# Kernel tuning notes

Measured on AMD Instinct MI355X. Metric: run time of the kernel, lower is better.

Reference implementation:

```python
import jax, jax.numpy as jnp
import numpy as np
from jax import lax

N = 63        # fixed by ConvTranspose chain: 3->5->9->17->33->63
ML = 3        # smoother mid channels
KS = 7        # smoother kernel size
MID = 32      # hypernet mid channels
K_ITERS = 5   # outer solver iterations
B = 256


def _conv2d(x, w, pad):
    return lax.conv_general_dilated(x, w, (1, 1), [(pad, pad), (pad, pad)],
                                    dimension_numbers=('NCHW', 'OIHW', 'NCHW'))


def _batch_conv2d(x, kernels):
    # per-sample 3x3 stencil conv via grouped conv: x [B,1,m,m], kernels [B,1,3,3]
    b, _, m1, m2 = x.shape
    out = lax.conv_general_dilated(x.reshape(1, b, m1, m2), kernels, (1, 1),
                                   [(0, 0), (0, 0)],
                                   dimension_numbers=('NCHW', 'OIHW', 'NCHW'),
                                   feature_group_count=b)
    return out.reshape(b, 1, m1 - 2, m2 - 2)


def _conv_transpose2d(x, w, b, stride, padding):
    # torch ConvTranspose2d: w layout [in, out, k, k]
    k = w.shape[-1]
    w2 = jnp.flip(w, (-2, -1)).transpose(1, 0, 2, 3)  # [out, in, k, k]
    p = k - 1 - padding
    y = lax.conv_general_dilated(x, w2, (1, 1), [(p, p), (p, p)],
                                 lhs_dilation=(stride, stride),
                                 dimension_numbers=('NCHW', 'OIHW', 'NCHW'))
    return y + b[None, :, None, None]


def _pad_bc(x):
    # F.pad (1,0,1,0) with 0 then (0,1,0,1) with 1
    x = jnp.pad(x, ((0, 0), (0, 0), (1, 0), (1, 0)))
    return jnp.pad(x, ((0, 0), (0, 0), (0, 1), (0, 1)), constant_values=1.0)


def _gelu(x):
    return jax.nn.gelu(x, approximate=False)  # torch nn.GELU default is exact


def setup_inputs() -> dict:
    key = jax.random.key(0)
    ks = jax.random.split(key, 24)
    s = 0.02
    d = {}
    d['x'] = jax.random.normal(ks[0], (B, 1, N, N), jnp.float32)
    d['f'] = jax.random.normal(ks[1], (B, 1, N, N), jnp.float32)
    d['kernelA'] = jax.random.normal(ks[2], (B, 1, 3, 3), jnp.float32)
    # smoother hypernetwork (two Linear(9->100->mL*ks*ks) stacks)
    d['fc1_w1'] = jax.random.normal(ks[3], (9, 100), jnp.float32) * s
    d['fc1_b1'] = jnp.zeros((100,), jnp.float32)
    d['fc1_w2'] = jax.random.normal(ks[4], (100, ML * KS * KS), jnp.float32) * s
    d['fc1_b2'] = jnp.zeros((ML * KS * KS,), jnp.float32)
    d['fc2_w1'] = jax.random.normal(ks[5], (9, 100), jnp.float32) * s
    d['fc2_b1'] = jnp.zeros((100,), jnp.float32)
    d['fc2_w2'] = jax.random.normal(ks[6], (100, ML * KS * KS), jnp.float32) * s
    d['fc2_b2'] = jnp.zeros((ML * KS * KS,), jnp.float32)
    # CNNFNS meta: 5 ConvTranspose2d layers (torch weight layout [in,out,k,k])
    d['ct1_w'] = jax.random.normal(ks[7], (1, MID, 3, 3), jnp.float32) * s
    d['ct1_b'] = jnp.zeros((MID,), jnp.float32)
    d['ct2_w'] = jax.random.normal(ks[8], (MID, MID, 3, 3), jnp.float32) * s
    d['ct2_b'] = jnp.zeros((MID,), jnp.float32)
    d['ct3_w'] = jax.random.normal(ks[9], (MID, MID, 3, 3), jnp.float32) * s
    d['ct3_b'] = jnp.zeros((MID,), jnp.float32)
    d['ct4_w'] = jax.random.normal(ks[10], (MID, MID, 3, 3), jnp.float32) * s
    d['ct4_b'] = jnp.zeros((MID,), jnp.float32)
    d['ct5_w'] = jax.random.normal(ks[11], (MID, 2, 3, 3), jnp.float32) * s
    d['ct5_b'] = jnp.zeros((2,), jnp.float32)
    return d


def reference(x, f, kernelA,
              fc1_w1, fc1_b1, fc1_w2, fc1_b2,
              fc2_w1, fc2_b1, fc2_w2, fc2_b2,
              ct1_w, ct1_b, ct2_w, ct2_b, ct3_w, ct3_b, ct4_w, ct4_b, ct5_w, ct5_b):
    bsz = x.shape[0]

    # --- hypernet weights depend only on kernelA: hoist out of the K loop ---
    flatA = kernelA.reshape(bsz, 9)
    w1 = (_gelu(flatA @ fc1_w1 + fc1_b1) @ fc1_w2 + fc1_b2).reshape(bsz, ML, 1, KS, KS)
    w2 = (_gelu(flatA @ fc2_w1 + fc2_b1) @ fc2_w2 + fc2_b2).reshape(bsz, 1, ML, KS, KS)

    h = _gelu(_conv_transpose2d(kernelA, ct1_w, ct1_b, 2, 1))
    h = _gelu(_conv_transpose2d(h, ct2_w, ct2_b, 2, 1))
    h = _gelu(_conv_transpose2d(h, ct3_w, ct3_b, 2, 1))
    h = _gelu(_conv_transpose2d(h, ct4_w, ct4_b, 2, 1))
    h = _conv_transpose2d(h, ct5_w, ct5_b, 2, 2)          # [B,2,N,N]
    hw = h.reshape(bsz, 1, N, N, 2)                        # memory-reinterp view as in torch
    wc = lax.complex(hw[..., 0], hw[..., 1])               # [B,1,N,N] complex

    def residual(xc):
        return f - _batch_conv2d(_pad_bc(xc), kernelA)

    def smoother(xc):
        r = residual(xc)
        def per(r_i, a_i, b_i):
            t = _conv2d(r_i[None], a_i, KS // 2)           # [1,ML,N,N]
            return _conv2d(t, b_i, KS // 2)[0]             # [1,N,N]
        g2 = jax.vmap(per)(r, w1, w2)
        return xc + g2

    def h_correct(r):
        r_hat = jnp.fft.fft2(r, norm='ortho')
        out_ft = r_hat * wc
        # torch irfft2(s=(N,N)) trims last dim to N//2+1
        return jnp.fft.irfft2(out_ft[..., : N // 2 + 1], s=(N, N), norm='ortho')

    for _ in range(K_ITERS):
        x = smoother(x)
        x = x + h_correct(residual(x))
    r = residual(x)
    return jnp.linalg.norm(r) / bsz
```

## Files before the change

kernel.cpp:

```cpp
#include <hip/hip_runtime.h>
#include <math.h>

#define NB   256
#define ND   63
#define NN   3969
#define WST  1028

__device__ __forceinline__ float gelu_f(float v){
    return 0.5f * v * (1.0f + erff(v * 0.70710678118654752440f));
}

#define FMA4(A, W, S) { (A).x=fmaf((W).x,(S),(A).x); (A).y=fmaf((W).y,(S),(A).y); \
                        (A).z=fmaf((W).z,(S),(A).z); (A).w=fmaf((W).w,(S),(A).w); }

union F4  { float4 v;    float a[4];  };
union W16 { float4 v[4]; float a[16]; };

__device__ __forceinline__ float4 gelu4(const F4& x){
    float4 r;
    r.x = gelu_f(x.a[0]); r.y = gelu_f(x.a[1]);
    r.z = gelu_f(x.a[2]); r.w = gelu_f(x.a[3]);
    return r;
}

__device__ __forceinline__ int dec_base(int uc, int H){
    int h2 = H >> 1;
    return (uc < h2) ? 4*uc : (uc < H) ? 4*(uc - h2) + 1 : 2*H;
}

template<int SIN, int SOUT, int OST, int NT>
__device__ __forceinline__ void ct_quad_stage(const float* __restrict__ cin,
                                              float* __restrict__ cout,
                                              const float* __restrict__ wb,
                                              const float* __restrict__ bsv,
                                              int tid){
    const int H  = (SOUT - 1) >> 1;
    const int UX = H + 1;
    const int NU = UX * UX * 8;
    for (int u = tid; u < NU; u += NT){
        const int cell = u >> 3, q = u & 7;
        const int ucy = cell / UX, ucx = cell - ucy*UX;
        const int oy = dec_base(ucy, H), ox = dec_base(ucx, H);
        const bool vx = (ox + 2 <= 2*H), vy = (oy + 2 <= 2*H);
        int nky, kyA[2], iyA[2];
        if (oy & 1){ nky=2; kyA[0]=0; iyA[0]=(oy+1)>>1; kyA[1]=2; iyA[1]=(oy-1)>>1; }
        else       { nky=1; kyA[0]=1; iyA[0]=oy>>1; kyA[1]=1; iyA[1]=0; }
        int nkx, kxA[2], ixA[2];
        if (ox & 1){ nkx=2; kxA[0]=0; ixA[0]=(ox+1)>>1; kxA[1]=2; ixA[1]=(ox-1)>>1; }
        else       { nkx=1; kxA[0]=1; ixA[0]=ox>>1; kxA[1]=1; ixA[1]=0; }
        F4 a00, a01, a10, a11;
        a00.v = ((const float4*)bsv)[q]; a01.v = a00.v; a10.v = a00.v; a11.v = a00.v;
        for (int yi = 0; yi < nky; yi++)
        for (int xi = 0; xi < nkx; xi++){
            const float* wp  = wb + (kyA[yi]*3 + kxA[xi])*WST + 4*q;
            const float* p00 = cin + (iyA[yi]*SIN + ixA[xi])*36;
            const float* p01 = p00 + 36;
            const float* p10 = p00 + SIN*36;
            const float* p11 = p10 + 36;
            #pragma unroll
            for (int g = 0; g < 8; g++){
                F4 i00, i01, i10, i11;
                i00.v = *(const float4*)(p00 + 4*g);
                i01.v = *(const float4*)(p01 + 4*g);
                i10.v = *(const float4*)(p10 + 4*g);
                i11.v = *(const float4*)(p11 + 4*g);
                #pragma unroll
                for (int cc = 0; cc < 4; cc++){
                    float4 w = *(const float4*)(wp + (4*g + cc)*32);
                    FMA4(a00.v, w, i00.a[cc]);
                    FMA4(a01.v, w, i01.a[cc]);
                    FMA4(a10.v, w, i10.a[cc]);
                    FMA4(a11.v, w, i11.a[cc]);
                }
            }
        }
        float4 g00 = gelu4(a00), g01 = gelu4(a01), g10 = gelu4(a10), g11 = gelu4(a11);
        size_t base = (size_t)(oy*SOUT + ox)*OST + 4*q;
        *(float4*)(cout + base) = g00;
        if (vx)        *(float4*)(cout + base + 2*(size_t)OST) = g01;
        if (vy)        *(float4*)(cout + base + 2*(size_t)SOUT*OST) = g10;
        if (vx && vy)  *(float4*)(cout + base + 2*(size_t)(SOUT+1)*OST) = g11;
    }
}

__global__ __launch_bounds__(1024)
__attribute__((amdgpu_waves_per_eu(4, 4)))
void k_ct1234(const float* __restrict__ kA,
              const float* __restrict__ cw1,
              const float* __restrict__ cw2,
              const float* __restrict__ cw3,
              const float* __restrict__ cw4,
              const float* __restrict__ b1,
              const float* __restrict__ b2,
              const float* __restrict__ b3,
              const float* __restrict__ b4,
              float* __restrict__ c4out,
              float* __restrict__ acc){
    __shared__ __align__(16) float wbuf[9*WST];
    __shared__ __align__(16) float w1s[9*36];
    __shared__ __align__(16) float c1s[31*36];
    __shared__ __align__(16) float c2s[91*36];
    __shared__ __align__(16) float c3s[307*36];
    __shared__ float b1s[32], b2s[32], b3s[32], b4s[32];
    const int b = blockIdx.x, tid = threadIdx.x;
    if (b == 0 && tid == 0) acc[0] = 0.f;
    for (int i = tid; i < 9216; i += 1024){
        int ci = i / 288, co = (i / 9) & 31, tap = i % 9;
        wbuf[tap*WST + ci*32 + co] = cw2[i];
    }
    if (tid < 288) w1s[(tid % 9)*36 + tid/9] = cw1[tid];
    if (tid < 32){ b1s[tid]=b1[tid]; b2s[tid]=b2[tid]; b3s[tid]=b3[tid]; b4s[tid]=b4[tid]; }
    __syncthreads();
    if (tid < 200){
        int px = tid >> 3, q = tid & 7;
        int oy = px / 5, ox = px % 5;
        F4 a4; a4.v = ((const float4*)b1s)[q];
        int nky, kyA[2], iyA[2];
        if (oy & 1){ nky=2; kyA[0]=0; iyA[0]=(oy+1)/2; kyA[1]=2; iyA[1]=(oy-1)/2; }
        else       { nky=1; kyA[0]=1; iyA[0]=oy/2; kyA[1]=1; iyA[1]=0; }
        int nkx, kxA[2], ixA[2];
        if (ox & 1){ nkx=2; kxA[0]=0; ixA[0]=(ox+1)/2; kxA[1]=2; ixA[1]=(ox-1)/2; }
        else       { nkx=1; kxA[0]=1; ixA[0]=ox/2; kxA[1]=1; ixA[1]=0; }
        const float* ab = kA + b*9;
        for (int yi = 0; yi < nky; yi++)
        for (int xi = 0; xi < nkx; xi++){
            float v = ab[iyA[yi]*3 + ixA[xi]];
            float4 w = *(const float4*)(w1s + (kyA[yi]*3 + kxA[xi])*36 + 4*q);
            FMA4(a4.v, w, v);
        }
        *(float4*)(c1s + px*36 + 4*q) = gelu4(a4);
    }
    __syncthreads();
    ct_quad_stage<5, 9, 36, 1024>(c1s, c2s, wbuf, b2s, tid);
    __syncthreads();
    for (int i = tid; i < 9216; i += 1024){
        int ci = i / 288, co = (i / 9) & 31, tap = i % 9;
        wbuf[tap*WST + ci*32 + co] = cw3[i];
    }
    __syncthreads();
    ct_quad_stage<9, 17, 36, 1024>(c2s, c3s, wbuf, b3s, tid);
    __syncthreads();
    for (int i = tid; i < 9216; i += 1024){
        int ci = i / 288, co = (i / 9) & 31, tap = i % 9;
        wbuf[tap*WST + ci*32 + co] = cw4[i];
    }
    __syncthreads();
    ct_quad_stage<17, 33, 32, 1024>(c3s, c4out + (size_t)b*(1089*32), wbuf, b4s, tid);
}

__global__ __launch_bounds__(512) void k_solve(const float* __restrict__ x0g,
                                               const float* __restrict__ f,
                                               const float* __restrict__ kAg,
                                               const float* __restrict__ w1a, const float* __restrict__ b1a,
                                               const float* __restrict__ w2a, const float* __restrict__ b2a,
                                               const float* __restrict__ w1b, const float* __restrict__ b1b,
                                               const float* __restrict__ w2b, const float* __restrict__ b2b,
                                               const float* __restrict__ cw5,
                                               const float* __restrict__ b5,
                                               const float* __restrict__ c4g,
                                               float* __restrict__ accg){
    __shared__ __align__(16) float xs[65*68 + 8];
    __shared__ __align__(16) float U[17152 + 8];
    __shared__ __align__(16) float Fs_r[32*68 + 8];
    __shared__ __align__(16) float Fs_i[32*68 + 8];
    __shared__ __align__(16) float vcs[4096];
    __shared__ float ws5b[9*68];
    __shared__ float w1s[148], w2s[148], dvs[64], ds_r[32], ds_i[32], red[8], hs[100];
    const int b = blockIdx.x, tid = threadIdx.x;
    float* rs  = U;
    float* tc0 = U + 4288;
    float* tc1 = U + 8576;
    float* tc2 = U + 12864;
    float*  rP  = U;
    const float4* rP4 = (const float4*)U;
    float2* TtC = (float2*)(U + 4352);
    float2* MC2 = (float2*)(U + 8448);
    float4* CC4 = (float4*)(U + 12544);
    float* c5s = U;
    const float4* F4r = (const float4*)Fs_r;
    const float4* F4i = (const float4*)Fs_i;
    const float4* vc4s = (const float4*)vcs;
    const float* fg = f + (size_t)b*NN;
    float ka[9];
    #pragma unroll
    for (int i = 0; i < 9; i++) ka[i] = kAg[b*9 + i];

    for (int i = tid; i < 2176; i += 512){
        int r = i / 68, c = i % 68;
        float vr = 0.f, vi = 0.f;
        if (c < 63){
            int m = (r * c) % 63;
            float ang = 6.283185307179586f * (float)m / 63.0f;
            vr = cosf(ang); vi = -sinf(ang);
        }
        Fs_r[i] = vr; Fs_i[i] = vi;
    }
    for (int i = tid; i < 4428; i += 512){
        int r = i / 68, c = i - r*68;
        bool interior = (r >= 1 && r <= 63 && c >= 4 && c <= 66);
        if (!interior) xs[i] = (r == 64 || c == 67) ? 1.f : 0.f;
    }
    for (int i = tid; i < 576; i += 512){
        int ci = i / 18, co = (i / 9) & 1, tap = i % 9;
        ws5b[tap*68 + ci*2 + co] = cw5[i];
    }
    for (int i = tid; i < NN; i += 512) xs[(i/ND + 1)*68 + (i%ND) + 4] = x0g[(size_t)b*NN + i];
    if (tid < 100){
        float s = b1a[tid];
        #pragma unroll
        for (int i = 0; i < 9; i++) s = fmaf(ka[i], w1a[i*100 + tid], s);
        hs[tid] = gelu_f(s);
    }
    __syncthreads();
    if (tid < 147){
        float s = b2a[tid];
        for (int k = 0; k < 100; k++) s = fmaf(hs[k], w2a[k*147 + tid], s);
        w1s[tid] = s;
    }
    __syncthreads();
    if (tid < 100){
        float s = b1b[tid];
        #pragma unroll
        for (int i = 0; i < 9; i++) s = fmaf(ka[i], w1b[i*100 + tid], s);
        hs[tid] = gelu_f(s);
    }
    __syncthreads();
    if (tid < 147){
        float s = b2b[tid];
        for (int k = 0; k < 100; k++) s = fmaf(hs[k], w2b[k*147 + tid], s);
        w2s[tid] = s;
    }
    {
        const float* ib = c4g + (size_t)b * (1089*32);
        float bb0 = b5[0], bb1 = b5[1];
        for (int p = tid; p < NN; p += 512){
            int oy = p / ND, ox = p % ND;
            float a0 = bb0, a1 = bb1;
            int nky, kyA[2], iyA[2];
            if ((oy & 1) == 0){ nky=2; kyA[0]=0; iyA[0]=oy/2+1; kyA[1]=2; iyA[1]=oy/2; }
            else              { nky=1; kyA[0]=1; iyA[0]=(oy+1)/2; kyA[1]=1; iyA[1]=0; }
            int nkx, kxA[2], ixA[2];
            if ((ox & 1) == 0){ nkx=2; kxA[0]=0; ixA[0]=ox/2+1; kxA[1]=2; ixA[1]=ox/2; }
            else              { nkx=1; kxA[0]=1; ixA[0]=(ox+1)/2; kxA[1]=1; ixA[1]=0; }
            for (int yi = 0; yi < nky; yi++)
            for (int xi = 0; xi < nkx; xi++){
                const float* ip = ib + ((size_t)iyA[yi]*33 + ixA[xi])*32;
                const float* wp = ws5b + (kyA[yi]*3 + kxA[xi])*68;
                #pragma unroll
                for (int g = 0; g < 8; g++){
                    F4 iv; iv.v = *(const float4*)(ip + 4*g);
                    #pragma unroll
                    for (int q = 0; q < 4; q++){
                        int ci = 4*g + q;
                        a0 = fmaf(iv.a[q], wp[ci*2],   a0);
                        a1 = fmaf(iv.a[q], wp[ci*2+1], a1);
                    }
                }
            }
            c5s[p]      = a0;
            c5s[NN + p] = a1;
        }
    }
    __syncthreads();
    {
        const float sc = 1.0f / 3969.0f;
        float4* vout = (float4*)vcs;
        for (int i = tid; i < 1024; i += 512){
            int ky = i >> 5, ct2 = i & 31;
            float4 o;
            #pragma unroll
            for (int j = 0; j < 2; j++){
                int kx = 2*ct2 + j;
                float re = 0.f, im = 0.f;
                if (kx <= 31){ int o2 = 2*(ky*ND + kx); re = c5s[o2]*sc; im = c5s[o2+1]*sc; }
                else if (kx <= 62){
                    int sy = (ND - ky) % ND, sx = ND - kx;
                    int o2 = 2*(sy*ND + sx); re = c5s[o2]*sc; im = -c5s[o2+1]*sc;
                }
                if (j == 0){ o.x = re; o.y = im; } else { o.z = re; o.w = im; }
            }
            vout[i] = o;
        }
        if (tid < 32){
            float2 d = {0.f, 0.f};
            if (tid >= 1){
                int iA = (ND - tid) * ND, iB = tid * ND;
                d.x = (c5s[2*iA]     - c5s[2*iB])     * sc;
                d.y = (c5s[2*iA + 1] + c5s[2*iB + 1]) * sc;
            }
            ((float2*)dvs)[tid] = d;
        }
    }
    __syncthreads();

    const int kt = tid >> 4, cg = tid & 15;
    const bool act = tid < 504;
    const int y0 = tid >> 3, xc = 8*(tid & 7);

    for (int it = 0; it < 5; it++){
        if (act){
            float racc[8] = {};
            #pragma unroll
            for (int dy = 0; dy < 3; dy++){
                W16 w;
                const float4* rp = (const float4*)(xs + (y0 + dy)*68 + xc);
                w.v[0]=rp[0]; w.v[1]=rp[1]; w.v[2]=rp[2]; w.v[3]=rp[3];
                #pragma unroll
                for (int dx = 0; dx < 3; dx++){
                    float kv = ka[dy*3 + dx];
                    #pragma unroll
                    for (int t = 0; t < 8; t++) racc[t] = fmaf(kv, w.a[3 + t + dx], racc[t]);
                }
            }
            int nw = 63 - xc; if (nw > 8) nw = 8;
            const float* fr_ = fg + y0*ND + xc;
            for (int t = 0; t < nw; t++) rs[y0*68 + 3 + xc + t] = fr_[t] - racc[t];
        }
        for (int i = tid; i < 1276; i += 512){
            int buf = i / 319, j = i - buf*319;
            float* base = U + buf*4288;
            int idx;
            if (j < 315){ int rr = j/5, cc = j - rr*5; idx = rr*68 + ((cc < 3) ? cc : 63 + cc); }
            else idx = 4284 + (j - 315);
            base[idx] = 0.f;
        }
        __syncthreads();
        if (act){
            float A0[8] = {}, A1[8] = {}, A2[8] = {};
            for (int dy = 0; dy < 7; dy++){
                int ry = y0 + dy - 3;
                if (ry < 0 || ry >= 63) continue;
                W16 w16;
                const float4* rp = (const float4*)(rs + ry*68 + xc);
                w16.v[0]=rp[0]; w16.v[1]=rp[1]; w16.v[2]=rp[2]; w16.v[3]=rp[3];
                #pragma unroll
                for (int dx = 0; dx < 7; dx++){
                    float w0 = w1s[dy*7 + dx];
                    float w1 = w1s[49 + dy*7 + dx];
                    float w2 = w1s[98 + dy*7 + dx];
                    #pragma unroll
                    for (int t = 0; t < 8; t++){
                        float v = w16.a[t+dx];
                        A0[t] = fmaf(w0, v, A0[t]);
                        A1[t] = fmaf(w1, v, A1[t]);
                        A2[t] = fmaf(w2, v, A2[t]);
                    }
                }
            }
            int nw = 63 - xc; if (nw > 8) nw = 8;
            for (int t = 0; t < nw; t++){
                int o = y0*68 + 3 + xc + t;
                tc0[o] = A0[t]; tc1[o] = A1[t]; tc2[o] = A2[t];
            }
        }
        __syncthreads();
        if (act){
            float acc2[8] = {};
            #pragma unroll
            for (int c = 0; c < 3; c++){
                const float* tcc = (c == 0) ? tc0 : (c == 1) ? tc1 : tc2;
                for (int dy = 0; dy < 7; dy++){
                    int ry = y0 + dy - 3;
                    if (ry < 0 || ry >= 63) continue;
                    W16 w16;
                    const float4* tp = (const float4*)(tcc + ry*68 + xc);
                    w16.v[0]=tp[0]; w16.v[1]=tp[1]; w16.v[2]=tp[2]; w16.v[3]=tp[3];
                    #pragma unroll
                    for (int dx = 0; dx < 7; dx++){
                        float wv = w2s[c*49 + dy*7 + dx];
                        #pragma unroll
                        for (int t = 0; t < 8; t++) acc2[t] = fmaf(wv, w16.a[t+dx], acc2[t]);
                    }
                }
            }
            int nw = 63 - xc; if (nw > 8) nw = 8;
            for (int t = 0; t < nw; t++) xs[(y0+1)*68 + 4 + xc + t] += acc2[t];
        }
        __syncthreads();
        if (act){
            float racc[8] = {};
            #pragma unroll
            for (int dy = 0; dy < 3; dy++){
                W16 w;
                const float4* rp = (const float4*)(xs + (y0 + dy)*68 + xc);
                w.v[0]=rp[0]; w.v[1]=rp[1]; w.v[2]=rp[2]; w.v[3]=rp[3];
                #pragma unroll
                for (int dx = 0; dx < 3; dx++){
                    float kv = ka[dy*3 + dx];
                    #pragma unroll
                    for (int t = 0; t < 8; t++) racc[t] = fmaf(kv, w.a[3 + t + dx], racc[t]);
                }
            }
            float out[8];
            #pragma unroll
            for (int t = 0; t < 8; t++){
                int ci = xc + t; if (ci > 62) ci = 62;
                float fv = fg[y0*ND + ci];
                out[t] = (xc + t < 63) ? (fv - racc[t]) : 0.f;
            }
            *(float4*)(rP + y0*68 + xc)     = make_float4(out[0],out[1],out[2],out[3]);
            *(float4*)(rP + y0*68 + xc + 4) = make_float4(out[4],out[5],out[6],out[7]);
        }
        __syncthreads();
        {
            float tr0,ti0=0.f,tr1,ti1=0.f,tr2,ti2=0.f,tr3,ti3=0.f;
            { F4 rv; rv.v = rP4[cg]; tr0=rv.a[0]; tr1=rv.a[1]; tr2=rv.a[2]; tr3=rv.a[3]; }
            #define A_PAIR(MM, JJ) { \
                F4 r1, r2; \
                r1.v = rP4[(MM)*17 + cg]; \
                r2.v = rP4[(63-(MM))*17 + cg]; \
                float fr = f4r.a[JJ], fi = f4i.a[JJ]; \
                float S0=r1.a[0]+r2.a[0], D0=r1.a[0]-r2.a[0]; \
                float S1=r1.a[1]+r2.a[1], D1=r1.a[1]-r2.a[1]; \
                float S2=r1.a[2]+r2.a[2], D2=r1.a[2]-r2.a[2]; \
                float S3=r1.a[3]+r2.a[3], D3=r1.a[3]-r2.a[3]; \
                tr0 = fmaf(fr, S0, tr0); ti0 = fmaf(fi, D0, ti0); \
                tr1 = fmaf(fr, S1, tr1); ti1 = fmaf(fi, D1, ti1); \
                tr2 = fmaf(fr, S2, tr2); ti2 = fmaf(fi, D2, ti2); \
                tr3 = fmaf(fr, S3, tr3); ti3 = fmaf(fi, D3, ti3); }
            {
                F4 f4r, f4i; f4r.v = F4r[kt*17]; f4i.v = F4i[kt*17];
                A_PAIR(1, 1) A_PAIR(2, 2) A_PAIR(3, 3)
            }
            for (int mq = 1; mq < 8; mq++){
                F4 f4r, f4i;
                f4r.v = F4r[kt*17 + mq];
                f4i.v = F4i[kt*17 + mq];
                A_PAIR(4*mq + 0, 0) A_PAIR(4*mq + 1, 1)
                A_PAIR(4*mq + 2, 2) A_PAIR(4*mq + 3, 3)
            }
            #undef A_PAIR
            const int c0 = 4*cg;
            TtC[(c0+0)*32 + ((kt + c0 + 0) & 31)] = make_float2(tr0, ti0);
            TtC[(c0+1)*32 + ((kt + c0 + 1) & 31)] = make_float2(tr1, ti1);
            TtC[(c0+2)*32 + ((kt + c0 + 2) & 31)] = make_float2(tr2, ti2);
            TtC[(c0+3)*32 + ((kt + c0 + 3) & 31)] = make_float2(tr3, ti3);
        }
        {
            float R0r,R0i,R1r,R1i,R2r,R2i,R3r,R3i;
            {
                float2 T0 = TtC[kt & 31];
                R0r = T0.x; R0i = T0.y;
                R1r = T0.x; R1i = T0.y;
                R2r = T0.x; R2i = T0.y;
                R3r = T0.x; R3i = T0.y;
            }
            for (int np = 1; np <= 31; np++){
                int n2 = 63 - np;
                float2 T1 = TtC[np*32 + ((kt + np) & 31)];
                float2 T2 = TtC[n2*32 + ((kt + n2) & 31)];
                F4 fr, fi;
                fr.v = F4r[np*17 + cg];
                fi.v = F4i[np*17 + cg];
                float Sx = T1.x + T2.x, Dx = T1.x - T2.x;
                float Sy = T1.y + T2.y, Dy = T2.y - T1.y;
                R0r = fmaf(fr.a[0], Sx, R0r); R0r = fmaf(fi.a[0], Dy, R0r);
                R0i = fmaf(fi.a[0], Dx, R0i); R0i = fmaf(fr.a[0], Sy, R0i);
                R1r = fmaf(fr.a[1], Sx, R1r); R1r = fmaf(fi.a[1], Dy, R1r);
                R1i = fmaf(fi.a[1], Dx, R1i); R1i = fmaf(fr.a[1], Sy, R1i);
                R2r = fmaf(fr.a[2], Sx, R2r); R2r = fmaf(fi.a[2], Dy, R2r);
                R2i = fmaf(fi.a[2], Dx, R2i); R2i = fmaf(fr.a[2], Sy, R2i);
                R3r = fmaf(fr.a[3], Sx, R3r); R3r = fmaf(fi.a[3], Dy, R3r);
                R3i = fmaf(fi.a[3], Dx, R3i); R3i = fmaf(fr.a[3], Sy, R3i);
            }
            if (cg == 0){
                float2 dv = ((const float2*)dvs)[kt];
                ds_r[kt] = R0r*dv.x + R0i*dv.y;
                ds_i[kt] = R0r*dv.y - R0i*dv.x;
            }
            float4 vA = vc4s[kt*32 + 2*cg];
            float4 vB = vc4s[kt*32 + 2*cg + 1];
            const int c0 = 4*cg, rot = kt;
            MC2[kt*64 + ((c0+0 + rot) & 63)] = make_float2(R0r*vA.x - R0i*vA.y, R0r*vA.y + R0i*vA.x);
            MC2[kt*64 + ((c0+1 + rot) & 63)] = make_float2(R1r*vA.z - R1i*vA.w, R1r*vA.w + R1i*vA.z);
            MC2[kt*64 + ((c0+2 + rot) & 63)] = make_float2(R2r*vB.x - R2i*vB.y, R2r*vB.y + R2i*vB.x);
            MC2[kt*64 + ((c0+3 + rot) & 63)] = make_float2(R3r*vB.z - R3i*vB.w, R3r*vB.w + R3i*vB.z);
        }
        {
            const int rot = kt;
            float C0r,C0i,C1r,C1i,C2r,C2i,C3r,C3i;
            {
                float2 M0 = MC2[kt*64 + (rot & 63)];
                C0r = M0.x; C0i = M0.y;
                C1r = M0.x; C1i = M0.y;
                C2r = M0.x; C2i = M0.y;
                C3r = M0.x; C3i = M0.y;
            }
            for (int lp = 1; lp <= 31; lp++){
                int l2 = 63 - lp;
                float2 M1 = MC2[kt*64 + ((lp + rot) & 63)];
                float2 M2 = MC2[kt*64 + ((l2 + rot) & 63)];
                F4 fr, fi;
                fr.v = F4r[lp*17 + cg];
                fi.v = F4i[lp*17 + cg];
                float SMx = M1.x + M2.x, DMx = M2.x - M1.x;
                float SMy = M1.y + M2.y, DMy = M1.y - M2.y;
                C0r = fmaf(fr.a[0], SMx, C0r); C0r = fmaf(fi.a[0], DMy, C0r);
                C0i = fmaf(fr.a[0], SMy, C0i); C0i = fmaf(fi.a[0], DMx, C0i);
                C1r = fmaf(fr.a[1], SMx, C1r); C1r = fmaf(fi.a[1], DMy, C1r);
                C1i = fmaf(fr.a[1], SMy, C1i); C1i = fmaf(fi.a[1], DMx, C1i);
                C2r = fmaf(fr.a[2], SMx, C2r); C2r = fmaf(fi.a[2], DMy, C2r);
                C2i = fmaf(fr.a[2], SMy, C2i); C2i = fmaf(fi.a[2], DMx, C2i);
                C3r = fmaf(fr.a[3], SMx, C3r); C3r = fmaf(fi.a[3], DMy, C3r);
                C3i = fmaf(fr.a[3], SMy, C3i); C3i = fmaf(fi.a[3], DMx, C3i);
            }
            float sc2 = (kt == 0) ? 0.5f : 1.0f;
            CC4[kt*33 + 2*cg]     = make_float4(C0r*sc2, C0i*sc2, C1r*sc2, C1i*sc2);
            CC4[kt*33 + 2*cg + 1] = make_float4(C2r*sc2, C2i*sc2, C3r*sc2, C3i*sc2);
        }
        __syncthreads();
        if (tid < 256){
            const int pr = tid >> 3, qb = tid & 7;
            float sr[8] = {}, si[8] = {};
            float er = 0.f, ei = 0.f;
            for (int nq = 0; nq < 8; nq++){
                F4 f4r, f4i;
                f4r.v = F4r[pr*17 + nq];
                f4i.v = F4i[pr*17 + nq];
                #pragma unroll
                for (int j = 0; j < 4; j++){
                    int n = 4*nq + j;
                    float fr = f4r.a[j], fi = f4i.a[j];
                    float4 cA = CC4[n*33 + qb];
                    float4 cB = CC4[n*33 + qb + 8];
                    float4 cC = CC4[n*33 + qb + 16];
                    float4 cD = CC4[n*33 + qb + 24];
                    sr[0]=fmaf(fr,cA.x,sr[0]); si[0]=fmaf(fi,cA.y,si[0]);
                    sr[1]=fmaf(fr,cA.z,sr[1]); si[1]=fmaf(fi,cA.w,si[1]);
                    sr[2]=fmaf(fr,cB.x,sr[2]); si[2]=fmaf(fi,cB.y,si[2]);
                    sr[3]=fmaf(fr,cB.z,sr[3]); si[3]=fmaf(fi,cB.w,si[3]);
                    sr[4]=fmaf(fr,cC.x,sr[4]); si[4]=fmaf(fi,cC.y,si[4]);
                    sr[5]=fmaf(fr,cC.z,sr[5]); si[5]=fmaf(fi,cC.w,si[5]);
                    sr[6]=fmaf(fr,cD.x,sr[6]); si[6]=fmaf(fi,cD.y,si[6]);
                    sr[7]=fmaf(fr,cD.z,sr[7]); si[7]=fmaf(fi,cD.w,si[7]);
                    er = fmaf(fr, ds_r[n], er); ei = fmaf(fi, ds_i[n], ei);
                }
            }
            {
                float e0 = er - ei;
                float* xrow = xs + (pr+1)*68 + 4;
                float2* xp0 = (float2*)(xrow + 2*qb);
                float2* xp1 = (float2*)(xrow + 2*qb + 16);
                float2* xp2 = (float2*)(xrow + 2*qb + 32);
                float2* xp3 = (float2*)(xrow + 2*qb + 48);
                float2 v0=*xp0, v1=*xp1, v2=*xp2, v3=*xp3;
                v0.x += 2.f*(sr[0]+si[0]) + e0; v0.y += 2.f*(sr[1]+si[1]) + e0;
                v1.x += 2.f*(sr[2]+si[2]) + e0; v1.y += 2.f*(sr[3]+si[3]) + e0;
                v2.x += 2.f*(sr[4]+si[4]) + e0; v2.y += 2.f*(sr[5]+si[5]) + e0;
                v3.x += 2.f*(sr[6]+si[6]) + e0; v3.y += 2.f*(sr[7]+si[7]) + e0;
                *xp0=v0; *xp1=v1; *xp2=v2; *xp3=v3;
            }
            if (pr > 0){
                float e1 = er + ei;
                float* xrow = xs + (63-pr+1)*68 + 4;
                float2* xp0 = (float2*)(xrow + 2*qb);
                float2* xp1 = (float2*)(xrow + 2*qb + 16);
                float2* xp2 = (float2*)(xrow + 2*qb + 32);
                float2* xp3 = (float2*)(xrow + 2*qb + 48);
                float2 v0=*xp0, v1=*xp1, v2=*xp2, v3=*xp3;
                v0.x += 2.f*(sr[0]-si[0]) + e1; v0.y += 2.f*(sr[1]-si[1]) + e1;
                v1.x += 2.f*(sr[2]-si[2]) + e1; v1.y += 2.f*(sr[3]-si[3]) + e1;
                v2.x += 2.f*(sr[4]-si[4]) + e1; v2.y += 2.f*(sr[5]-si[5]) + e1;
                v3.x += 2.f*(sr[6]-si[6]) + e1; v3.y += 2.f*(sr[7]-si[7]) + e1;
                *xp0=v0; *xp1=v1; *xp2=v2; *xp3=v3;
            }
        }
        __syncthreads();
    }
    float s = 0.f;
    if (act){
        float racc[8] = {};
        #pragma unroll
        for (int dy = 0; dy < 3; dy++){
            W16 w;
            const float4* rp = (const float4*)(xs + (y0 + dy)*68 + xc);
            w.v[0]=rp[0]; w.v[1]=rp[1]; w.v[2]=rp[2]; w.v[3]=rp[3];
            #pragma unroll
            for (int dx = 0; dx < 3; dx++){
                float kv = ka[dy*3 + dx];
                #pragma unroll
                for (int t = 0; t < 8; t++) racc[t] = fmaf(kv, w.a[3 + t + dx], racc[t]);
            }
        }
        #pragma unroll
        for (int t = 0; t < 8; t++){
            if (xc + t < 63){
                float r = fg[y0*ND + xc + t] - racc[t];
                s = fmaf(r, r, s);
            }
        }
    }
    #pragma unroll
    for (int off = 32; off > 0; off >>= 1) s += __shfl_down(s, off, 64);
    int lane = tid & 63, w = tid >> 6;
    if (lane == 0) red[w] = s;
    __syncthreads();
    if (tid == 0){
        float t = 0.f;
        #pragma unroll
        for (int i = 0; i < 8; i++) t += red[i];
        atomicAdd(accg, t);
    }
}

__global__ void k_final(const float* __restrict__ acc, float* __restrict__ out){
    if (threadIdx.x == 0 && blockIdx.x == 0) out[0] = sqrtf(acc[0]) * (1.0f/256.0f);
}

extern "C" void kernel_launch(void* const* d_in, const int* in_sizes, int n_in,
                              void* d_out, int out_size, void* d_ws, size_t ws_size,
                              hipStream_t stream){
    const float* x0     = (const float*)d_in[0];
    const float* f      = (const float*)d_in[1];
    const float* kA     = (const float*)d_in[2];
    const float* fc1_w1 = (const float*)d_in[3];
    const float* fc1_b1 = (const float*)d_in[4];
    const float* fc1_w2 = (const float*)d_in[5];
    const float* fc1_b2 = (const float*)d_in[6];
    const float* fc2_w1 = (const float*)d_in[7];
    const float* fc2_b1 = (const float*)d_in[8];
    const float* fc2_w2 = (const float*)d_in[9];
    const float* fc2_b2 = (const float*)d_in[10];
    const float* ct1_w  = (const float*)d_in[11];
    const float* ct1_b  = (const float*)d_in[12];
    const float* ct2_w  = (const float*)d_in[13];
    const float* ct2_b  = (const float*)d_in[14];
    const float* ct3_w  = (const float*)d_in[15];
    const float* ct3_b  = (const float*)d_in[16];
    const float* ct4_w  = (const float*)d_in[17];
    const float* ct4_b  = (const float*)d_in[18];
    const float* ct5_w  = (const float*)d_in[19];
    const float* ct5_b  = (const float*)d_in[20];
    float* out = (float*)d_out;

    float* ws = (float*)d_ws;
    size_t off = 0;
    auto take = [&](size_t n){ float* p = ws + off; off += (n + 63) & ~(size_t)63; return p; };
    float* acc = take(64);
    float* c4  = take((size_t)NB*32*1089);
    (void)ws_size; (void)in_sizes; (void)n_in; (void)out_size;

    k_ct1234<<<NB, 1024, 0, stream>>>(kA, ct1_w, ct2_w, ct3_w, ct4_w,
                                      ct1_b, ct2_b, ct3_b, ct4_b, c4, acc);
    k_solve<<<NB, 512, 0, stream>>>(x0, f, kA,
                                    fc1_w1, fc1_b1, fc1_w2, fc1_b2,
                                    fc2_w1, fc2_b1, fc2_w2, fc2_b2,
                                    ct5_w, ct5_b, c4, acc);
    k_final<<<1, 64, 0, stream>>>(acc, out);
}
```

Measured before the change: 326.0 us.

## Split last transposed-conv stage into separate kernel with two blocks per sample

After: 334.3 us. 1.03x slower.

```diff
diff --git a/kernel.cpp b/kernel.cpp
--- a/kernel.cpp
+++ b/kernel.cpp
@@ -33,11 +33,12 @@
                                               float* __restrict__ cout,
                                               const float* __restrict__ wb,
                                               const float* __restrict__ bsv,
-                                              int tid){
+                                              int tid, int u0, int u1){
     const int H  = (SOUT - 1) >> 1;
     const int UX = H + 1;
     const int NU = UX * UX * 8;
-    for (int u = tid; u < NU; u += NT){
+    if (u1 > NU) u1 = NU;
+    for (int u = u0 + tid; u < u1; u += NT){
         const int cell = u >> 3, q = u & 7;
         const int ucy = cell / UX, ucx = cell - ucy*UX;
         const int oy = dec_base(ucy, H), ox = dec_base(ucx, H);
@@ -85,23 +86,21 @@
 
 __global__ __launch_bounds__(1024)
 __attribute__((amdgpu_waves_per_eu(4, 4)))
-void k_ct1234(const float* __restrict__ kA,
-              const float* __restrict__ cw1,
-              const float* __restrict__ cw2,
-              const float* __restrict__ cw3,
-              const float* __restrict__ cw4,
-              const float* __restrict__ b1,
-              const float* __restrict__ b2,
-              const float* __restrict__ b3,
-              const float* __restrict__ b4,
-              float* __restrict__ c4out,
-              float* __restrict__ acc){
+void k_ct123(const float* __restrict__ kA,
+             const float* __restrict__ cw1,
+             const float* __restrict__ cw2,
+             const float* __restrict__ cw3,
+             const float* __restrict__ b1,
+             const float* __restrict__ b2,
+             const float* __restrict__ b3,
+             float* __restrict__ c3out,
+             float* __restrict__ acc){
     __shared__ __align__(16) float wbuf[9*WST];
     __shared__ __align__(16) float w1s[9*36];
     __shared__ __align__(16) float c1s[31*36];
     __shared__ __align__(16) float c2s[91*36];
     __shared__ __align__(16) float c3s[307*36];
-    __shared__ float b1s[32], b2s[32], b3s[32], b4s[32];
+    __shared__ float b1s[32], b2s[32], b3s[32];
     const int b = blockIdx.x, tid = threadIdx.x;
     if (b == 0 && tid == 0) acc[0] = 0.f;
     for (int i = tid; i < 9216; i += 1024){
@@ -109,7 +108,7 @@
         wbuf[tap*WST + ci*32 + co] = cw2[i];
     }
     if (tid < 288) w1s[(tid % 9)*36 + tid/9] = cw1[tid];
-    if (tid < 32){ b1s[tid]=b1[tid]; b2s[tid]=b2[tid]; b3s[tid]=b3[tid]; b4s[tid]=b4[tid]; }
+    if (tid < 32){ b1s[tid]=b1[tid]; b2s[tid]=b2[tid]; b3s[tid]=b3[tid]; }
     __syncthreads();
     if (tid < 200){
         int px = tid >> 3, q = tid & 7;
@@ -131,21 +130,38 @@
         *(float4*)(c1s + px*36 + 4*q) = gelu4(a4);
     }
     __syncthreads();
-    ct_quad_stage<5, 9, 36, 1024>(c1s, c2s, wbuf, b2s, tid);
+    ct_quad_stage<5, 9, 36, 1024>(c1s, c2s, wbuf, b2s, tid, 0, 1<<30);
     __syncthreads();
     for (int i = tid; i < 9216; i += 1024){
         int ci = i / 288, co = (i / 9) & 31, tap = i % 9;
         wbuf[tap*WST + ci*32 + co] = cw3[i];
     }
     __syncthreads();
-    ct_quad_stage<9, 17, 36, 1024>(c2s, c3s, wbuf, b3s, tid);
-    __syncthreads();
-    for (int i = tid; i < 9216; i += 1024){
+    ct_quad_stage<9, 17, 36, 1024>(c2s, c3s, wbuf, b3s, tid, 0, 1<<30);
+    __syncthreads();
+    float* cg = c3out + (size_t)b * 9248;
+    for (int i = tid; i < 9248; i += 1024) cg[i] = c3s[(i >> 5)*36 + (i & 31)];
+}
+
+__global__ __launch_bounds__(512) void k_ct4(const float* __restrict__ c3g,
+                                             const float* __restrict__ cw4,
+                                             const float* __restrict__ b4,
+                                             float* __restrict__ c4out){
+    __shared__ __align__(16) float wbuf[9*WST];
+    __shared__ __align__(16) float c3s[307*36];
+    __shared__ float b4s[32];
+    const int sample = blockIdx.x >> 1, half = blockIdx.x & 1, tid = threadIdx.x;
+    for (int i = tid; i < 9216; i += 512){
         int ci = i / 288, co = (i / 9) & 31, tap = i % 9;
         wbuf[tap*WST + ci*32 + co] = cw4[i];
     }
-    __syncthreads();
-    ct_quad_stage<17, 33, 32, 1024>(c3s, c4out + (size_t)b*(1089*32), wbuf, b4s, tid);
+    const float* cg = c3g + (size_t)sample * 9248;
+    for (int i = tid; i < 9248; i += 512) c3s[(i >> 5)*36 + (i & 31)] = cg[i];
+    for (int i = tid; i < 307*36 - 289*36; i += 512) c3s[289*36 + i] = 0.f;
+    if (tid < 32) b4s[tid] = b4[tid];
+    __syncthreads();
+    ct_quad_stage<17, 33, 32, 512>(c3s, c4out + (size_t)sample*(1089*32), wbuf, b4s,
+                                   tid, half*1156, half*1156 + 1156);
 }
 
 __global__ __launch_bounds__(512) void k_solve(const float* __restrict__ x0g,
@@ -638,10 +654,12 @@
     auto take = [&](size_t n){ float* p = ws + off; off += (n + 63) & ~(size_t)63; return p; };
     float* acc = take(64);
     float* c4  = take((size_t)NB*32*1089);
+    float* c3  = take((size_t)NB*9248);
     (void)ws_size; (void)in_sizes; (void)n_in; (void)out_size;
 
-    k_ct1234<<<NB, 1024, 0, stream>>>(kA, ct1_w, ct2_w, ct3_w, ct4_w,
-                                      ct1_b, ct2_b, ct3_b, ct4_b, c4, acc);
+    k_ct123<<<NB, 1024, 0, stream>>>(kA, ct1_w, ct2_w, ct3_w,
+                                     ct1_b, ct2_b, ct3_b, c3, acc);
+    k_ct4<<<NB*2, 512, 0, stream>>>(c3, ct4_w, ct4_b, c4);
     k_solve<<<NB, 512, 0, stream>>>(x0, f, kA,
                                     fc1_w1, fc1_b1, fc1_w2, fc1_b2,
                                     fc2_w1, fc2_b1, fc2_w2, fc2_b2,
```
